# Kernel tuning notes

Hardware: AMD Instinct MI355X
Metric: run time of the kernel (lower is better)

The kernel has to match this reference:

```python
import jax, jax.numpy as jnp
import numpy as np

KQ = 512
NEG = -1e9


def setup_inputs() -> dict:
    key = jax.random.key(0)
    k1, k2, k3, k4, k5 = jax.random.split(key, 5)
    B, NQ, NK, D, V, O = 16, 1024, 2048, 512, 512, 256
    return {
        "keys": jax.random.normal(k1, (B, NK, D), dtype=jnp.float32),
        "queries": jax.random.normal(k2, (B, NQ, D), dtype=jnp.float32),
        "values": jax.random.normal(k3, (B, NK, V), dtype=jnp.float32),
        "mask": jax.random.randint(k4, (B, NQ, NK), 0, 2, dtype=jnp.int32),
        "W_resize": jax.random.normal(k5, (O, V), dtype=jnp.float32) * (1.0 / np.sqrt(V)),
        "b_resize": jnp.zeros((O,), dtype=jnp.float32),
    }


def reference(keys, queries, values, mask, W_resize, b_resize):
    # score: scaled dot product  [B, NQ, NK]
    logits = jnp.einsum("bqd,bkd->bqk", queries, keys) / jnp.sqrt(jnp.float32(KQ))
    logits = jnp.where(mask == 0, jnp.float32(NEG), logits)
    attn = jax.nn.softmax(logits, axis=-1)
    # context: [B, NQ, V]
    context = jnp.einsum("bqk,bkv->bqv", attn, values)
    # resize to out_size
    context = jnp.einsum("bqv,ov->bqo", context, W_resize) + b_resize
    return context
```

## Files before the change

kernel.cpp:

```cpp
#include <hip/hip_runtime.h>

#define BB   16
#define NQ   1024
#define NK   2048
#define DD   512
#define VV   512
#define OO   256
#define SCALE 0.044194173824159216f

typedef __attribute__((ext_vector_type(4))) float f32x4;
typedef __attribute__((ext_vector_type(8))) short s16x8;

#define AS1(p) ((const __attribute__((address_space(1))) void*)(p))
#define AS3(p) ((__attribute__((address_space(3))) void*)(p))

__device__ __forceinline__ unsigned short f2bf(float f) {
  unsigned u = __float_as_uint(f);
  u += 0x7fffu + ((u >> 16) & 1u);
  return (unsigned short)(u >> 16);
}
__device__ __forceinline__ float bf2f(unsigned short b) {
  return __uint_as_float(((unsigned)b) << 16);
}

#define MFMA16(a, b, c) __builtin_amdgcn_mfma_f32_16x16x32_bf16(a, b, c, 0, 0, 0)

__device__ __forceinline__ void gemm_bt_core(
    const unsigned short* __restrict__ Abase,
    const unsigned short* __restrict__ Bbase,
    int K,
    unsigned short* smem,
    f32x4 acc[4][4])
{
  const int t = threadIdx.x;
  const int w = t >> 6;
  const int l = t & 63;
  const int srow = l >> 2;
  const int scol = (l & 3) * 8;
  const int r0 = (w * 2 + 0) * 16 + srow;
  const int r1 = (w * 2 + 1) * 16 + srow;
  const int ld0 = (w * 2 + 0) * 512 + l * 8;
  const int ld1 = (w * 2 + 1) * 512 + l * 8;
  const int wm = (w >> 1) * 64;
  const int wn = (w & 1) * 64;
  const int lm = l & 15;
  const int lq = l >> 4;

#define QK_STAGE(buf, kt) do {                                                             \
    unsigned short* As_ = smem + (buf) * 8192;                                             \
    unsigned short* Bs_ = As_ + 4096;                                                      \
    __builtin_amdgcn_global_load_lds(AS1(Abase + (size_t)r0 * K + (kt) + scol), AS3(As_ + ld0), 16, 0, 0); \
    __builtin_amdgcn_global_load_lds(AS1(Abase + (size_t)r1 * K + (kt) + scol), AS3(As_ + ld1), 16, 0, 0); \
    __builtin_amdgcn_global_load_lds(AS1(Bbase + (size_t)r0 * K + (kt) + scol), AS3(Bs_ + ld0), 16, 0, 0); \
    __builtin_amdgcn_global_load_lds(AS1(Bbase + (size_t)r1 * K + (kt) + scol), AS3(Bs_ + ld1), 16, 0, 0); \
  } while (0)

  QK_STAGE(0, 0);
  __syncthreads();
  for (int kt = 0; kt < K; kt += 32) {
    const int cur = (kt >> 5) & 1;
    if (kt + 32 < K) QK_STAGE(cur ^ 1, kt + 32);
    const unsigned short* As = smem + cur * 8192;
    const unsigned short* Bs = As + 4096;
    s16x8 af[4], bfr[4];
    #pragma unroll
    for (int i = 0; i < 4; ++i) {
      af[i]  = *(const s16x8*)(As + (wm + i * 16 + lm) * 32 + lq * 8);
      bfr[i] = *(const s16x8*)(Bs + (wn + i * 16 + lm) * 32 + lq * 8);
    }
    #pragma unroll
    for (int mi = 0; mi < 4; ++mi)
      #pragma unroll
      for (int ni = 0; ni < 4; ++ni)
        acc[mi][ni] = MFMA16(af[mi], bfr[ni], acc[mi][ni]);
    __syncthreads();
  }
#undef QK_STAGE
}


#define CS_STRIDE 136

__global__ __launch_bounds__(256)
void qkvw_kernel(const unsigned short* __restrict__ Qb,
                 const unsigned short* __restrict__ Kb,
                 const unsigned short* __restrict__ Vb,
                 const unsigned short* __restrict__ Wb,
                 const int* __restrict__ mask,
                 unsigned short* __restrict__ P,
                 unsigned short* __restrict__ VWt,
                 float* __restrict__ sums)
{
  __shared__ unsigned short smem[17408];
  unsigned short* Cs = smem;
  const int bid = blockIdx.x;
  const int t = threadIdx.x, w = t >> 6, l = t & 63;
  const int wm = (w >> 1) * 64, wn = (w & 1) * 64;
  const int lm = l & 15, lq = l >> 4;
  const int trow = t >> 4, tcol = (t & 15) * 8;

  f32x4 acc[4][4];
  #pragma unroll
  for (int i = 0; i < 4; ++i)
    #pragma unroll
    for (int j = 0; j < 4; ++j) acc[i][j] = (f32x4){0.f, 0.f, 0.f, 0.f};

  if (bid < 2048) {
    const int b  = bid >> 7;
    const int tm = (bid >> 4) & 7;
    const int tn = bid & 15;

    gemm_bt_core(Qb + ((size_t)b * NQ + tm * 128) * DD,
                 Kb + ((size_t)b * NK + tn * 128) * DD, DD, smem, acc);

    #pragma unroll
    for (int mi = 0; mi < 4; ++mi)
      #pragma unroll
      for (int ni = 0; ni < 4; ++ni)
        #pragma unroll
        for (int r = 0; r < 4; ++r)
          Cs[(wm + mi * 16 + lq * 4 + r) * CS_STRIDE + wn + ni * 16 + lm] =
              f2bf(acc[mi][ni][r] * SCALE);
    __syncthreads();

    #pragma unroll
    for (int it = 0; it < 8; ++it) {
      const int row = it * 16 + trow;
      const int gq = tm * 128 + row;
      const size_t gbase = ((size_t)b * NQ + gq) * NK + tn * 128 + tcol;
      s16x8 v = *(const s16x8*)(Cs + row * CS_STRIDE + tcol);
      const int4 m0 = *(const int4*)(mask + gbase);
      const int4 m1 = *(const int4*)(mask + gbase + 4);
      float e[8];
      e[0] = m0.x ? __expf(bf2f((unsigned short)v[0])) : 0.f;
      e[1] = m0.y ? __expf(bf2f((unsigned short)v[1])) : 0.f;
      e[2] = m0.z ? __expf(bf2f((unsigned short)v[2])) : 0.f;
      e[3] = m0.w ? __expf(bf2f((unsigned short)v[3])) : 0.f;
      e[4] = m1.x ? __expf(bf2f((unsigned short)v[4])) : 0.f;
      e[5] = m1.y ? __expf(bf2f((unsigned short)v[5])) : 0.f;
      e[6] = m1.z ? __expf(bf2f((unsigned short)v[6])) : 0.f;
      e[7] = m1.w ? __expf(bf2f((unsigned short)v[7])) : 0.f;
      float sp = 0.f;
      #pragma unroll
      for (int j = 0; j < 8; ++j) sp += e[j];
      #pragma unroll
      for (int off = 8; off > 0; off >>= 1) sp += __shfl_down(sp, off, 16);
      if ((t & 15) == 0) atomicAdd(&sums[(size_t)b * NQ + gq], sp);
      s16x8 o;
      #pragma unroll
      for (int j = 0; j < 8; ++j) o[j] = (short)f2bf(e[j]);
      *(s16x8*)(P + gbase) = o;
    }
  } else {
    const int vid = bid - 2048;
    const int b  = vid >> 5;
    const int kt = (vid >> 1) & 15;
    const int ot = vid & 1;

    gemm_bt_core(Vb + ((size_t)b * NK + kt * 128) * VV,
                 Wb + (size_t)ot * 128 * VV, VV, smem, acc);

    #pragma unroll
    for (int mi = 0; mi < 4; ++mi)
      #pragma unroll
      for (int ni = 0; ni < 4; ++ni)
        #pragma unroll
        for (int r = 0; r < 4; ++r)
          Cs[(wn + ni * 16 + lm) * CS_STRIDE + wm + mi * 16 + lq * 4 + r] =
              f2bf(acc[mi][ni][r]);
    __syncthreads();

    #pragma unroll
    for (int it = 0; it < 8; ++it) {
      const int orow = it * 16 + trow;
      s16x8 v = *(const s16x8*)(Cs + orow * CS_STRIDE + tcol);
      *(s16x8*)(VWt + ((size_t)b * OO + ot * 128 + orow) * NK + kt * 128 + tcol) = v;
    }
  }
}

#define PW_STRIDE 132
__global__ __launch_bounds__(256)
void pvw_kernel(const unsigned short* __restrict__ P,
                const unsigned short* __restrict__ VWt,
                const float* __restrict__ sums,
                const float* __restrict__ bias,
                float* __restrict__ out)
{
  const int ot = blockIdx.x;
  const int qt = blockIdx.y;
  const int b  = blockIdx.z;
  __shared__ unsigned short smem[24576];
  __shared__ float Ls[64];

  const int t = threadIdx.x, w = t >> 6, l = t & 63;
  const int wr = w >> 1, wc = w & 1;
  const int lm = l & 15, lq = l >> 4;
  if (t < 64) Ls[t] = 1.0f / sums[(size_t)b * NQ + qt * 64 + t];

  f32x4 acc[2][4];
  #pragma unroll
  for (int i = 0; i < 2; ++i)
    #pragma unroll
    for (int j = 0; j < 4; ++j) acc[i][j] = (f32x4){0.f, 0.f, 0.f, 0.f};

  const unsigned short* Abase = P   + ((size_t)b * NQ + qt * 64) * NK;
  const unsigned short* Bbase = VWt + ((size_t)b * OO + ot * 128) * NK;

  const int srow = t >> 3;
  const int ssc  = (((t & 7) ^ (srow & 7)) << 3);

#define PV_STAGE(buf, k0v) do {                                                            \
    unsigned short* As_ = smem + (buf) * 12288;                                            \
    unsigned short* Bs_ = As_ + 4096;                                                      \
    const int k0_ = (k0v);                                                                 \
    __builtin_amdgcn_global_load_lds(AS1(Abase + (size_t)(srow     ) * NK + k0_ + ssc), AS3(As_ +        t * 8), 16, 0, 0); \
    __builtin_amdgcn_global_load_lds(AS1(Abase + (size_t)(srow + 32) * NK + k0_ + ssc), AS3(As_ + 2048 + t * 8), 16, 0, 0); \
    __builtin_amdgcn_global_load_lds(AS1(Bbase + (size_t)(srow     ) * NK + k0_ + ssc), AS3(Bs_ +        t * 8), 16, 0, 0); \
    __builtin_amdgcn_global_load_lds(AS1(Bbase + (size_t)(srow + 32) * NK + k0_ + ssc), AS3(Bs_ + 2048 + t * 8), 16, 0, 0); \
    __builtin_amdgcn_global_load_lds(AS1(Bbase + (size_t)(srow + 64) * NK + k0_ + ssc), AS3(Bs_ + 4096 + t * 8), 16, 0, 0); \
    __builtin_amdgcn_global_load_lds(AS1(Bbase + (size_t)(srow + 96) * NK + k0_ + ssc), AS3(Bs_ + 6144 + t * 8), 16, 0, 0); \
  } while (0)

  PV_STAGE(0, 0);
  __syncthreads();
  for (int k0 = 0; k0 < NK; k0 += 64) {
    const int cur = (k0 >> 6) & 1;
    if (k0 + 64 < NK) PV_STAGE(cur ^ 1, k0 + 64);
    const unsigned short* As = smem + cur * 12288;
    const unsigned short* Bs = As + 4096;
    s16x8 af[2][2], bfr[4][2];
    #pragma unroll
    for (int mi = 0; mi < 2; ++mi) {
      const int row = wr * 32 + mi * 16 + lm;
      #pragma unroll
      for (int ks = 0; ks < 2; ++ks)
        af[mi][ks] = *(const s16x8*)(As + row * 64 + (((ks * 4 + lq) ^ (row & 7)) << 3));
    }
    #pragma unroll
    for (int ni = 0; ni < 4; ++ni) {
      const int row = wc * 64 + ni * 16 + lm;
      #pragma unroll
      for (int ks = 0; ks < 2; ++ks)
        bfr[ni][ks] = *(const s16x8*)(Bs + row * 64 + (((ks * 4 + lq) ^ (row & 7)) << 3));
    }
    #pragma unroll
    for (int mi = 0; mi < 2; ++mi)
      #pragma unroll
      for (int ni = 0; ni < 4; ++ni) {
        acc[mi][ni] = MFMA16(af[mi][0], bfr[ni][0], acc[mi][ni]);
        acc[mi][ni] = MFMA16(af[mi][1], bfr[ni][1], acc[mi][ni]);
      }
    __syncthreads();
  }
#undef PV_STAGE

  float* Csf = (float*)smem;
  #pragma unroll
  for (int mi = 0; mi < 2; ++mi)
    #pragma unroll
    for (int ni = 0; ni < 4; ++ni)
      #pragma unroll
      for (int r = 0; r < 4; ++r) {
        const int row = wr * 32 + mi * 16 + lq * 4 + r;
        const int col = wc * 64 + ni * 16 + lm;
        Csf[row * PW_STRIDE + col] = acc[mi][ni][r] * Ls[row];
      }
  __syncthreads();
  const int trow = t >> 2;
  #pragma unroll
  for (int it = 0; it < 4; ++it) {
    const int col = (t & 3) * 8 + it * 32;
    f32x4 a = *(const f32x4*)(Csf + trow * PW_STRIDE + col);
    f32x4 c = *(const f32x4*)(Csf + trow * PW_STRIDE + col + 4);
    const int go = ot * 128 + col;
    a += *(const f32x4*)(bias + go);
    c += *(const f32x4*)(bias + go + 4);
    float* o = out + ((size_t)b * NQ + qt * 64 + trow) * OO + go;
    *(f32x4*)o = a;
    *(f32x4*)(o + 4) = c;
  }
}

__device__ __forceinline__ void cvt8(const float* __restrict__ in,
                                     unsigned short* __restrict__ out, int i)
{
  const float4* p = (const float4*)in + (size_t)i * 2;
  const float4 a = p[0], b = p[1];
  s16x8 o;
  o[0] = (short)f2bf(a.x); o[1] = (short)f2bf(a.y);
  o[2] = (short)f2bf(a.z); o[3] = (short)f2bf(a.w);
  o[4] = (short)f2bf(b.x); o[5] = (short)f2bf(b.y);
  o[6] = (short)f2bf(b.z); o[7] = (short)f2bf(b.w);
  ((s16x8*)out)[i] = o;
}

__global__ __launch_bounds__(256)
void prep_kernel(const float* __restrict__ q, const float* __restrict__ k,
                 const float* __restrict__ v, const float* __restrict__ w,
                 unsigned short* __restrict__ Qb, unsigned short* __restrict__ Kb,
                 unsigned short* __restrict__ Vb, unsigned short* __restrict__ Wb,
                 float* __restrict__ sums)
{
  const int bid = blockIdx.x;
  const int t = threadIdx.x;
  if (bid < 4096) {
    cvt8(q, Qb, bid * 256 + t);
  } else if (bid < 12288) {
    cvt8(k, Kb, (bid - 4096) * 256 + t);
  } else if (bid < 20480) {
    cvt8(v, Vb, (bid - 12288) * 256 + t);
  } else if (bid < 20544) {
    cvt8(w, Wb, (bid - 20480) * 256 + t);
  } else {
    const int i = (bid - 20544) * 256 + t;
    if (i < BB * NQ) sums[i] = 0.f;
  }
}

extern "C" void kernel_launch(void* const* d_in, const int* in_sizes, int n_in,
                              void* d_out, int out_size, void* d_ws, size_t ws_size,
                              hipStream_t stream)
{
  const float* keys    = (const float*)d_in[0];
  const float* queries = (const float*)d_in[1];
  const float* values  = (const float*)d_in[2];
  const int*   mask    = (const int*)  d_in[3];
  const float* W       = (const float*)d_in[4];
  const float* bias    = (const float*)d_in[5];
  float* out = (float*)d_out;

  char* ws = (char*)d_ws;
  unsigned short* Qb  = (unsigned short*)(ws);
  unsigned short* Kb  = (unsigned short*)(ws + (16ull << 20));
  unsigned short* Vb  = (unsigned short*)(ws + (48ull << 20));
  unsigned short* Wb  = (unsigned short*)(ws + (80ull << 20));
  unsigned short* VWt = (unsigned short*)(ws + (81ull << 20));
  unsigned short* P   = (unsigned short*)(ws + (97ull << 20));
  float* sums         = (float*)(ws + (161ull << 20));

  prep_kernel<<<dim3(20608), 256, 0, stream>>>(queries, keys, values, W,
                                               Qb, Kb, Vb, Wb, sums);
  qkvw_kernel<<<dim3(2560), 256, 0, stream>>>(Qb, Kb, Vb, Wb, mask, P, VWt, sums);
  pvw_kernel<<<dim3(OO / 128, NQ / 64, BB), 256, 0, stream>>>(P, VWt, sums, bias, out);
}
```

Before: 417.2 us.

## Drop double buffering in GEMM core and coarsen prep conversion blocks

```diff
diff --git a/kernel.cpp b/kernel.cpp
--- a/kernel.cpp
+++ b/kernel.cpp
@@ -29,7 +29,7 @@
     const unsigned short* __restrict__ Abase,
     const unsigned short* __restrict__ Bbase,
     int K,
-    unsigned short* smem,
+    unsigned short* As, unsigned short* Bs,
     f32x4 acc[4][4])
 {
   const int t = threadIdx.x;
@@ -39,29 +39,19 @@
   const int scol = (l & 3) * 8;
   const int r0 = (w * 2 + 0) * 16 + srow;
   const int r1 = (w * 2 + 1) * 16 + srow;
-  const int ld0 = (w * 2 + 0) * 512 + l * 8;
-  const int ld1 = (w * 2 + 1) * 512 + l * 8;
+  const int lds0 = (w * 2 + 0) * 512 + l * 8;
+  const int lds1 = (w * 2 + 1) * 512 + l * 8;
   const int wm = (w >> 1) * 64;
   const int wn = (w & 1) * 64;
   const int lm = l & 15;
   const int lq = l >> 4;
 
-#define QK_STAGE(buf, kt) do {                                                             \
-    unsigned short* As_ = smem + (buf) * 8192;                                             \
-    unsigned short* Bs_ = As_ + 4096;                                                      \
-    __builtin_amdgcn_global_load_lds(AS1(Abase + (size_t)r0 * K + (kt) + scol), AS3(As_ + ld0), 16, 0, 0); \
-    __builtin_amdgcn_global_load_lds(AS1(Abase + (size_t)r1 * K + (kt) + scol), AS3(As_ + ld1), 16, 0, 0); \
-    __builtin_amdgcn_global_load_lds(AS1(Bbase + (size_t)r0 * K + (kt) + scol), AS3(Bs_ + ld0), 16, 0, 0); \
-    __builtin_amdgcn_global_load_lds(AS1(Bbase + (size_t)r1 * K + (kt) + scol), AS3(Bs_ + ld1), 16, 0, 0); \
-  } while (0)
-
-  QK_STAGE(0, 0);
-  __syncthreads();
   for (int kt = 0; kt < K; kt += 32) {
-    const int cur = (kt >> 5) & 1;
-    if (kt + 32 < K) QK_STAGE(cur ^ 1, kt + 32);
-    const unsigned short* As = smem + cur * 8192;
-    const unsigned short* Bs = As + 4096;
+    __builtin_amdgcn_global_load_lds(AS1(Abase + (size_t)r0 * K + kt + scol), AS3(As + lds0), 16, 0, 0);
+    __builtin_amdgcn_global_load_lds(AS1(Abase + (size_t)r1 * K + kt + scol), AS3(As + lds1), 16, 0, 0);
+    __builtin_amdgcn_global_load_lds(AS1(Bbase + (size_t)r0 * K + kt + scol), AS3(Bs + lds0), 16, 0, 0);
+    __builtin_amdgcn_global_load_lds(AS1(Bbase + (size_t)r1 * K + kt + scol), AS3(Bs + lds1), 16, 0, 0);
+    __syncthreads();
     s16x8 af[4], bfr[4];
     #pragma unroll
     for (int i = 0; i < 4; ++i) {
@@ -75,7 +65,6 @@
         acc[mi][ni] = MFMA16(af[mi], bfr[ni], acc[mi][ni]);
     __syncthreads();
   }
-#undef QK_STAGE
 }
 
 
@@ -91,7 +80,9 @@
                  unsigned short* __restrict__ VWt,
                  float* __restrict__ sums)
 {
-  __shared__ unsigned short smem[17408];
+  __shared__ unsigned short smem[128 * CS_STRIDE];
+  unsigned short* As = smem;
+  unsigned short* Bs = smem + 4096;
   unsigned short* Cs = smem;
   const int bid = blockIdx.x;
   const int t = threadIdx.x, w = t >> 6, l = t & 63;
@@ -111,7 +102,7 @@
     const int tn = bid & 15;
 
     gemm_bt_core(Qb + ((size_t)b * NQ + tm * 128) * DD,
-                 Kb + ((size_t)b * NK + tn * 128) * DD, DD, smem, acc);
+                 Kb + ((size_t)b * NK + tn * 128) * DD, DD, As, Bs, acc);
 
     #pragma unroll
     for (int mi = 0; mi < 4; ++mi)
@@ -158,7 +149,7 @@
     const int ot = vid & 1;
 
     gemm_bt_core(Vb + ((size_t)b * NK + kt * 128) * VV,
-                 Wb + (size_t)ot * 128 * VV, VV, smem, acc);
+                 Wb + (size_t)ot * 128 * VV, VV, As, Bs, acc);
 
     #pragma unroll
     for (int mi = 0; mi < 4; ++mi)
@@ -304,17 +295,25 @@
 {
   const int bid = blockIdx.x;
   const int t = threadIdx.x;
-  if (bid < 4096) {
-    cvt8(q, Qb, bid * 256 + t);
-  } else if (bid < 12288) {
-    cvt8(k, Kb, (bid - 4096) * 256 + t);
-  } else if (bid < 20480) {
-    cvt8(v, Vb, (bid - 12288) * 256 + t);
-  } else if (bid < 20544) {
-    cvt8(w, Wb, (bid - 20480) * 256 + t);
+  if (bid < 1024) {
+    const int g0 = bid * 1024 + t;
+    #pragma unroll
+    for (int it = 0; it < 4; ++it) cvt8(q, Qb, g0 + it * 256);
+  } else if (bid < 3072) {
+    const int g0 = (bid - 1024) * 1024 + t;
+    #pragma unroll
+    for (int it = 0; it < 4; ++it) cvt8(k, Kb, g0 + it * 256);
+  } else if (bid < 5120) {
+    const int g0 = (bid - 3072) * 1024 + t;
+    #pragma unroll
+    for (int it = 0; it < 4; ++it) cvt8(v, Vb, g0 + it * 256);
+  } else if (bid < 5136) {
+    const int g0 = (bid - 5120) * 1024 + t;
+    #pragma unroll
+    for (int it = 0; it < 4; ++it) cvt8(w, Wb, g0 + it * 256);
   } else {
-    const int i = (bid - 20544) * 256 + t;
-    if (i < BB * NQ) sums[i] = 0.f;
+    const int i = (bid - 5136) * 1024 + t * 4;
+    *(float4*)(sums + i) = (float4){0.f, 0.f, 0.f, 0.f};
   }
 }
 
@@ -339,8 +338,8 @@
   unsigned short* P   = (unsigned short*)(ws + (97ull << 20));
   float* sums         = (float*)(ws + (161ull << 20));
 
-  prep_kernel<<<dim3(20608), 256, 0, stream>>>(queries, keys, values, W,
-                                               Qb, Kb, Vb, Wb, sums);
+  prep_kernel<<<dim3(5152), 256, 0, stream>>>(queries, keys, values, W,
+                                              Qb, Kb, Vb, Wb, sums);
   qkvw_kernel<<<dim3(2560), 256, 0, stream>>>(Qb, Kb, Vb, Wb, mask, P, VWt, sums);
   pvw_kernel<<<dim3(OO / 128, NQ / 64, BB), 256, 0, stream>>>(P, VWt, sums, bias, out);
 }
```

Measured after the change: 424.6 us. About the same (+1.8%).
